# Performance work log

Hardware: AMD Instinct MI355X
Metric: run time of the kernel (lower is better)

The kernel has to match this reference:

```python
import jax, jax.numpy as jnp
import numpy as np


def setup_inputs() -> dict:
    key = jax.random.key(0)
    k1, k2, k3, k4, k5 = jax.random.split(key, 5)
    B, T, H_enc, H_dec, A = 64, 2048, 512, 512, 512
    scale_enc = float(np.sqrt(2.0 / (H_enc + A)))  # xavier_uniform-ish scale
    scale_dec = float(np.sqrt(2.0 / (H_dec + A)))
    scale_v = float(np.sqrt(2.0 / (A + 1)))
    return {
        "encoder_outputs": jax.random.normal(k1, (B, T, H_enc), dtype=jnp.float32),
        "decoder_hidden": jax.random.normal(k2, (B, H_dec), dtype=jnp.float32),
        "W_enc": jax.random.normal(k3, (A, H_enc), dtype=jnp.float32) * scale_enc,
        "W_dec": jax.random.normal(k4, (A, H_dec), dtype=jnp.float32) * scale_dec,
        "V": jax.random.normal(k5, (1, A), dtype=jnp.float32) * scale_v,
    }


def reference(encoder_outputs, decoder_hidden, W_enc, W_dec, V):
    # enc_proj: [B,T,A]; dec_proj: [B,1,A] broadcast-added
    enc_proj = jnp.einsum("bth,ah->bta", encoder_outputs, W_enc)
    dec_proj = jnp.einsum("bh,ah->ba", decoder_hidden, W_dec)[:, None, :]
    energy = jnp.tanh(enc_proj + dec_proj)                      # [B,T,A]
    scores = jnp.einsum("bta,a->bt", energy, V[0])              # [B,T]
    attention_weights = jax.nn.softmax(scores, axis=1)          # [B,T]
    context_vector = jnp.einsum("bt,bth->bh", attention_weights, encoder_outputs)
    return context_vector, attention_weights
```

## Files before the change

kernel.cpp:

```cpp
#include <hip/hip_runtime.h>

#define B_ 64
#define T_ 2048
#define H_ 512
#define A_ 512

typedef unsigned short u16;
typedef __attribute__((ext_vector_type(8))) short bf16x8;
typedef __attribute__((ext_vector_type(4))) float f32x4;

__device__ __forceinline__ u16 f2bf(float f) {
  unsigned u = __float_as_uint(f);
  unsigned r = (u + 0x7FFFu + ((u >> 16) & 1u)) >> 16;
  return (u16)r;
}

__device__ __forceinline__ float bf2f(u16 h) {
  return __uint_as_float(((unsigned)h) << 16);
}

__device__ __forceinline__ float fast_tanh(float x) {
  float e = __expf(2.0f * x);
  return 1.0f - 2.0f * __builtin_amdgcn_rcpf(e + 1.0f);
}

__global__ void k_prep(const float* __restrict__ W, u16* __restrict__ wsB,
                       const float* __restrict__ dec, const float* __restrict__ Wd,
                       float* __restrict__ dp) {
  __shared__ float dl[H_];
  int tid = threadIdx.x;
  int bx = blockIdx.x;
  if (bx < 128) {
    int u = bx * 256 + tid;
    int a = u >> 6;
    int hq = u & 63;
    int ks = hq >> 2;
    int q = hq & 3;
    const float4* src = (const float4*)(W + a * H_ + hq * 8);
    float4 x0 = src[0], x1 = src[1];
    uint4 pk;
    pk.x = (unsigned)f2bf(x0.x) | ((unsigned)f2bf(x0.y) << 16);
    pk.y = (unsigned)f2bf(x0.z) | ((unsigned)f2bf(x0.w) << 16);
    pk.z = (unsigned)f2bf(x1.x) | ((unsigned)f2bf(x1.y) << 16);
    pk.w = (unsigned)f2bf(x1.z) | ((unsigned)f2bf(x1.w) << 16);
    int dst = ks * 2048 + (a >> 4) * 64 + q * 16 + (a & 15);
    ((uint4*)wsB)[dst] = pk;
  } else {
    int e = bx - 128;
    int b = e >> 3;
    int a0 = (e & 7) * 64;
    dl[tid] = dec[b * H_ + tid];
    dl[tid + 256] = dec[b * H_ + tid + 256];
    __syncthreads();
    int al = tid >> 2, p = tid & 3;
    const float4* wr = (const float4*)(Wd + (a0 + al) * H_ + p * 128);
    const float4* dv = (const float4*)(dl + p * 128);
    float s = 0.f;
#pragma unroll 8
    for (int i = 0; i < 32; ++i) {
      float4 w4 = wr[i], d4 = dv[i];
      s += w4.x * d4.x + w4.y * d4.y + w4.z * d4.z + w4.w * d4.w;
    }
    s += __shfl_xor(s, 1);
    s += __shfl_xor(s, 2);
    if (p == 0) dp[b * H_ + a0 + al] = s;
  }
}

__launch_bounds__(512, 4)
__global__ void k_scores(const float* __restrict__ enc, const u16* __restrict__ wsB,
                         const float* __restrict__ dpj, const float* __restrict__ V,
                         float* __restrict__ scores, float* __restrict__ part,
                         float* __restrict__ mz) {
  __shared__ __attribute__((aligned(16))) u16 Ab[64 * 512];
  __shared__ float red[8][64];
  __shared__ float e_lds[64];
  int tid = threadIdx.x;
  int w = tid >> 6, l = tid & 63;
  int q = l >> 4, r = l & 15;
  int m0 = blockIdx.x * 64;
  int b = m0 >> 11;

  int rem = tid & 255;
  int sm = rem >> 6, sq = (rem >> 4) & 3, sr = rem & 15;
  const float* ab = enc + (size_t)(m0 + sm * 16 + sr) * H_ + (tid >> 8) * 32 + sq * 8;

#define STG_WRITE(y0, y1, it)                                         \
  {                                                                   \
    uint4 pk;                                                         \
    pk.x = (unsigned)f2bf(y0.x) | ((unsigned)f2bf(y0.y) << 16);       \
    pk.y = (unsigned)f2bf(y0.z) | ((unsigned)f2bf(y0.w) << 16);       \
    pk.z = (unsigned)f2bf(y1.x) | ((unsigned)f2bf(y1.y) << 16);       \
    pk.w = (unsigned)f2bf(y1.z) | ((unsigned)f2bf(y1.w) << 16);       \
    ((uint4*)Ab)[(it) * 512 + tid] = pk;                              \
  }

  f32x4 acc[4][4];
#pragma unroll
  for (int m = 0; m < 4; ++m)
#pragma unroll
    for (int n = 0; n < 4; ++n) acc[m][n] = (f32x4){0.f, 0.f, 0.f, 0.f};

  const bf16x8* bfrag = (const bf16x8*)wsB;

  {
    float4 y0 = *((const float4*)(ab + 0));
    float4 y1 = *((const float4*)(ab + 4));
    float4 y2 = *((const float4*)(ab + 64));
    float4 y3 = *((const float4*)(ab + 68));
    STG_WRITE(y0, y1, 0)
    STG_WRITE(y2, y3, 1)
  }
  __syncthreads();

#pragma unroll
  for (int c = 0; c < 4; ++c) {
    float4 y0, y1, y2, y3;
    if (c < 3) {
      y0 = *((const float4*)(ab + (2 * c + 2) * 64));
      y1 = *((const float4*)(ab + (2 * c + 2) * 64 + 4));
      y2 = *((const float4*)(ab + (2 * c + 3) * 64));
      y3 = *((const float4*)(ab + (2 * c + 3) * 64 + 4));
    }
#pragma unroll
    for (int kk = 0; kk < 4; ++kk) {
      int ks = c * 4 + kk;
      bf16x8 bb[4], af[4];
#pragma unroll
      for (int n = 0; n < 4; ++n)
        bb[n] = bfrag[ks * 2048 + (w * 4 + n) * 64 + l];
#pragma unroll
      for (int m = 0; m < 4; ++m)
        af[m] = *((const bf16x8*)&Ab[(ks * 256 + m * 64 + l) * 8]);
      __builtin_amdgcn_s_setprio(1);
#pragma unroll
      for (int m = 0; m < 4; ++m)
#pragma unroll
        for (int n = 0; n < 4; ++n)
          acc[m][n] = __builtin_amdgcn_mfma_f32_16x16x32_bf16(af[m], bb[n], acc[m][n], 0, 0, 0);
      __builtin_amdgcn_s_setprio(0);
    }
    if (c < 3) {
      STG_WRITE(y0, y1, 2 * c + 2)
      STG_WRITE(y2, y3, 2 * c + 3)
    }
    __syncthreads();
  }

  float sp[4][4] = {};
  const float* db = dpj + b * A_;
#pragma unroll
  for (int n = 0; n < 4; ++n) {
    int col = w * 64 + n * 16 + r;
    float vv = V[col];
    float dd = db[col];
#pragma unroll
    for (int m = 0; m < 4; ++m)
#pragma unroll
      for (int j = 0; j < 4; ++j)
        sp[m][j] = fmaf(vv, fast_tanh(acc[m][n][j] + dd), sp[m][j]);
  }
#pragma unroll
  for (int m = 0; m < 4; ++m)
#pragma unroll
    for (int j = 0; j < 4; ++j) {
      float v = sp[m][j];
      v += __shfl_xor(v, 1);
      v += __shfl_xor(v, 2);
      v += __shfl_xor(v, 4);
      v += __shfl_xor(v, 8);
      sp[m][j] = v;
    }
  float outv = 0.f;
#pragma unroll
  for (int mm = 0; mm < 4; ++mm)
#pragma unroll
    for (int jj = 0; jj < 4; ++jj)
      if (r == mm * 4 + jj) outv = sp[mm][jj];
  red[w][(r >> 2) * 16 + q * 4 + (r & 3)] = outv;
  __syncthreads();

  if (tid < 64) {
    float s = 0.f;
#pragma unroll
    for (int ww = 0; ww < 8; ++ww) s += red[ww][tid];
    scores[m0 + tid] = s;
    float mx = s;
#pragma unroll
    for (int off = 1; off <= 32; off <<= 1) mx = fmaxf(mx, __shfl_xor(mx, off));
    float e = __expf(s - mx);
    float Z = e;
#pragma unroll
    for (int off = 1; off <= 32; off <<= 1) Z += __shfl_xor(Z, off);
    e_lds[tid] = e;
    if (tid == 0) {
      mz[blockIdx.x * 2] = mx;
      mz[blockIdx.x * 2 + 1] = Z;
    }
  }
  __syncthreads();

  {
    float pv0[8], pv1[8];
#pragma unroll
    for (int j = 0; j < 8; ++j) { pv0[j] = 0.f; pv1[j] = 0.f; }
#pragma unroll
    for (int ksl = 0; ksl < 2; ++ksl) {
      int ks = 2 * w + ksl;
#pragma unroll
      for (int m = 0; m < 4; ++m) {
        uint4 pk = ((const uint4*)Ab)[ks * 256 + m * 64 + l];
        float er = e_lds[m * 16 + r];
        float v0 = bf2f((u16)(pk.x & 0xffff)), v1 = bf2f((u16)(pk.x >> 16));
        float v2 = bf2f((u16)(pk.y & 0xffff)), v3 = bf2f((u16)(pk.y >> 16));
        float v4 = bf2f((u16)(pk.z & 0xffff)), v5 = bf2f((u16)(pk.z >> 16));
        float v6 = bf2f((u16)(pk.w & 0xffff)), v7 = bf2f((u16)(pk.w >> 16));
        if (ksl == 0) {
          pv0[0] = fmaf(er, v0, pv0[0]); pv0[1] = fmaf(er, v1, pv0[1]);
          pv0[2] = fmaf(er, v2, pv0[2]); pv0[3] = fmaf(er, v3, pv0[3]);
          pv0[4] = fmaf(er, v4, pv0[4]); pv0[5] = fmaf(er, v5, pv0[5]);
          pv0[6] = fmaf(er, v6, pv0[6]); pv0[7] = fmaf(er, v7, pv0[7]);
        } else {
          pv1[0] = fmaf(er, v0, pv1[0]); pv1[1] = fmaf(er, v1, pv1[1]);
          pv1[2] = fmaf(er, v2, pv1[2]); pv1[3] = fmaf(er, v3, pv1[3]);
          pv1[4] = fmaf(er, v4, pv1[4]); pv1[5] = fmaf(er, v5, pv1[5]);
          pv1[6] = fmaf(er, v6, pv1[6]); pv1[7] = fmaf(er, v7, pv1[7]);
        }
      }
    }
#pragma unroll
    for (int j = 0; j < 8; ++j) {
      float a0 = pv0[j], a1 = pv1[j];
      a0 += __shfl_xor(a0, 1); a1 += __shfl_xor(a1, 1);
      a0 += __shfl_xor(a0, 2); a1 += __shfl_xor(a1, 2);
      a0 += __shfl_xor(a0, 4); a1 += __shfl_xor(a1, 4);
      a0 += __shfl_xor(a0, 8); a1 += __shfl_xor(a1, 8);
      pv0[j] = a0; pv1[j] = a1;
    }
    float ov = 0.f;
#pragma unroll
    for (int jj = 0; jj < 8; ++jj) {
      if (r == jj) ov = pv0[jj];
      if (r == jj + 8) ov = pv1[jj];
    }
    int col = w * 64 + (r >> 3) * 32 + q * 8 + (r & 7);
    part[(size_t)blockIdx.x * 512 + col] = ov;
  }
#undef STG_WRITE
}

__global__ void k_softmax(const float* __restrict__ scores, float* __restrict__ wts) {
  __shared__ float rm[4], rs[4];
  int b = blockIdx.x, tid = threadIdx.x;
  float s[8];
#pragma unroll
  for (int i = 0; i < 8; ++i) s[i] = scores[b * T_ + i * 256 + tid];
  float mx = s[0];
#pragma unroll
  for (int i = 1; i < 8; ++i) mx = fmaxf(mx, s[i]);
#pragma unroll
  for (int off = 1; off <= 32; off <<= 1) mx = fmaxf(mx, __shfl_xor(mx, off));
  if ((tid & 63) == 0) rm[tid >> 6] = mx;
  __syncthreads();
  mx = fmaxf(fmaxf(rm[0], rm[1]), fmaxf(rm[2], rm[3]));
  float ex[8], se = 0.f;
#pragma unroll
  for (int i = 0; i < 8; ++i) { ex[i] = __expf(s[i] - mx); se += ex[i]; }
#pragma unroll
  for (int off = 1; off <= 32; off <<= 1) se += __shfl_xor(se, off);
  if ((tid & 63) == 0) rs[tid >> 6] = se;
  __syncthreads();
  se = rs[0] + rs[1] + rs[2] + rs[3];
  float inv = 1.0f / se;
#pragma unroll
  for (int i = 0; i < 8; ++i) wts[b * T_ + i * 256 + tid] = ex[i] * inv;
}

__global__ void k_ctx_comb(const float* __restrict__ part, const float* __restrict__ mz,
                           float* __restrict__ ctx) {
  __shared__ float sM[32], sZ[32];
  int b = blockIdx.x, tid = threadIdx.x;
  if (tid < 32) {
    sM[tid] = mz[(b * 32 + tid) * 2];
    sZ[tid] = mz[(b * 32 + tid) * 2 + 1];
  }
  __syncthreads();
  float M = sM[0];
#pragma unroll
  for (int i = 1; i < 32; ++i) M = fmaxf(M, sM[i]);
  float denom = 0.f;
#pragma unroll
  for (int i = 0; i < 32; ++i) denom += sZ[i] * __expf(sM[i] - M);
  float s = 0.f;
#pragma unroll
  for (int i = 0; i < 32; ++i)
    s += part[((size_t)b * 32 + i) * 512 + tid] * __expf(sM[i] - M);
  ctx[b * 512 + tid] = s / denom;
}

extern "C" void kernel_launch(void* const* d_in, const int* in_sizes, int n_in,
                              void* d_out, int out_size, void* d_ws, size_t ws_size,
                              hipStream_t stream) {
  const float* enc  = (const float*)d_in[0];
  const float* dec  = (const float*)d_in[1];
  const float* Wenc = (const float*)d_in[2];
  const float* Wdec = (const float*)d_in[3];
  const float* V    = (const float*)d_in[4];
  float* out = (float*)d_out;
  char* ws = (char*)d_ws;

  u16* wsB      = (u16*)ws;
  float* dpj    = (float*)(ws + 512 * 1024);
  float* scores = (float*)(ws + 640 * 1024);
  float* part   = (float*)(ws + 1152 * 1024);
  float* mz     = (float*)(ws + 1152 * 1024 + 4 * 1024 * 1024);

  float* ctx = out;
  float* wts = out + B_ * H_;

  hipLaunchKernelGGL(k_prep, dim3(640), dim3(256), 0, stream, Wenc, wsB, dec, Wdec, dpj);
  hipLaunchKernelGGL(k_scores, dim3(2048), dim3(512), 0, stream, enc, wsB, dpj, V,
                     scores, part, mz);
  hipLaunchKernelGGL(k_softmax, dim3(64), dim3(256), 0, stream, scores, wts);
  hipLaunchKernelGGL(k_ctx_comb, dim3(64), dim3(512), 0, stream, part, mz, ctx);
}
```

Baseline: 122.8 us.

## Deepen encoder staging prefetch and make all waves compute the softmax tail redundantly

The k_scores main loop now keeps two chunks of encoder loads in flight. Each chunk's global loads are issued two stages ahead of its LDS write, so global latency has more time to hide behind the MFMA work. __syncthreads is replaced with a raw lgkmcnt wait plus s_barrier, which skips waiting on outstanding vector-memory loads. The per-block max/exp reduction is computed redundantly by every wave, and the values are shared by shuffles instead of through an LDS buffer, which removes one barrier. The trade-off is higher register pressure from the extra prefetched float4s and duplicated transcendental work in every wave.

```diff
diff --git a/kernel.cpp b/kernel.cpp
--- a/kernel.cpp
+++ b/kernel.cpp
@@ -23,6 +23,8 @@
   float e = __expf(2.0f * x);
   return 1.0f - 2.0f * __builtin_amdgcn_rcpf(e + 1.0f);
 }
+
+#define BAR_LDS() asm volatile("s_waitcnt lgkmcnt(0)\n\ts_barrier" ::: "memory")
 
 __global__ void k_prep(const float* __restrict__ W, u16* __restrict__ wsB,
                        const float* __restrict__ dec, const float* __restrict__ Wd,
@@ -74,7 +76,6 @@
                          float* __restrict__ mz) {
   __shared__ __attribute__((aligned(16))) u16 Ab[64 * 512];
   __shared__ float red[8][64];
-  __shared__ float e_lds[64];
   int tid = threadIdx.x;
   int w = tid >> 6, l = tid & 63;
   int q = l >> 4, r = l & 15;
@@ -85,6 +86,13 @@
   int sm = rem >> 6, sq = (rem >> 4) & 3, sr = rem & 15;
   const float* ab = enc + (size_t)(m0 + sm * 16 + sr) * H_ + (tid >> 8) * 32 + sq * 8;
 
+#define LOADC(y0, y1, y2, y3, c)                                      \
+  {                                                                   \
+    y0 = *((const float4*)(ab + (2 * (c)) * 64));                     \
+    y1 = *((const float4*)(ab + (2 * (c)) * 64 + 4));                 \
+    y2 = *((const float4*)(ab + (2 * (c) + 1) * 64));                 \
+    y3 = *((const float4*)(ab + (2 * (c) + 1) * 64 + 4));             \
+  }
 #define STG_WRITE(y0, y1, it)                                         \
   {                                                                   \
     uint4 pk;                                                         \
@@ -94,6 +102,28 @@
     pk.w = (unsigned)f2bf(y1.z) | ((unsigned)f2bf(y1.w) << 16);       \
     ((uint4*)Ab)[(it) * 512 + tid] = pk;                              \
   }
+#define WRITEC(y0, y1, y2, y3, c)                                     \
+  {                                                                   \
+    STG_WRITE(y0, y1, 2 * (c))                                        \
+    STG_WRITE(y2, y3, 2 * (c) + 1)                                    \
+  }
+#define COMPUTE4(c)                                                   \
+  {                                                                   \
+    _Pragma("unroll") for (int kk = 0; kk < 4; ++kk) {                \
+      int ks = (c) * 4 + kk;                                          \
+      bf16x8 bb[4], af[4];                                            \
+      _Pragma("unroll") for (int n = 0; n < 4; ++n)                   \
+          bb[n] = bfrag[ks * 2048 + (w * 4 + n) * 64 + l];            \
+      _Pragma("unroll") for (int m = 0; m < 4; ++m)                   \
+          af[m] = *((const bf16x8*)&Ab[(ks * 256 + m * 64 + l) * 8]); \
+      __builtin_amdgcn_s_setprio(1);                                  \
+      _Pragma("unroll") for (int m = 0; m < 4; ++m)                   \
+          _Pragma("unroll") for (int n = 0; n < 4; ++n)               \
+              acc[m][n] = __builtin_amdgcn_mfma_f32_16x16x32_bf16(    \
+                  af[m], bb[n], acc[m][n], 0, 0, 0);                  \
+      __builtin_amdgcn_s_setprio(0);                                  \
+    }                                                                 \
+  }
 
   f32x4 acc[4][4];
 #pragma unroll
@@ -103,49 +133,23 @@
 
   const bf16x8* bfrag = (const bf16x8*)wsB;
 
-  {
-    float4 y0 = *((const float4*)(ab + 0));
-    float4 y1 = *((const float4*)(ab + 4));
-    float4 y2 = *((const float4*)(ab + 64));
-    float4 y3 = *((const float4*)(ab + 68));
-    STG_WRITE(y0, y1, 0)
-    STG_WRITE(y2, y3, 1)
-  }
-  __syncthreads();
-
-#pragma unroll
-  for (int c = 0; c < 4; ++c) {
-    float4 y0, y1, y2, y3;
-    if (c < 3) {
-      y0 = *((const float4*)(ab + (2 * c + 2) * 64));
-      y1 = *((const float4*)(ab + (2 * c + 2) * 64 + 4));
-      y2 = *((const float4*)(ab + (2 * c + 3) * 64));
-      y3 = *((const float4*)(ab + (2 * c + 3) * 64 + 4));
-    }
-#pragma unroll
-    for (int kk = 0; kk < 4; ++kk) {
-      int ks = c * 4 + kk;
-      bf16x8 bb[4], af[4];
-#pragma unroll
-      for (int n = 0; n < 4; ++n)
-        bb[n] = bfrag[ks * 2048 + (w * 4 + n) * 64 + l];
-#pragma unroll
-      for (int m = 0; m < 4; ++m)
-        af[m] = *((const bf16x8*)&Ab[(ks * 256 + m * 64 + l) * 8]);
-      __builtin_amdgcn_s_setprio(1);
-#pragma unroll
-      for (int m = 0; m < 4; ++m)
-#pragma unroll
-        for (int n = 0; n < 4; ++n)
-          acc[m][n] = __builtin_amdgcn_mfma_f32_16x16x32_bf16(af[m], bb[n], acc[m][n], 0, 0, 0);
-      __builtin_amdgcn_s_setprio(0);
-    }
-    if (c < 3) {
-      STG_WRITE(y0, y1, 2 * c + 2)
-      STG_WRITE(y2, y3, 2 * c + 3)
-    }
-    __syncthreads();
-  }
+  float4 ya0, ya1, ya2, ya3, yb0, yb1, yb2, yb3;
+  LOADC(ya0, ya1, ya2, ya3, 0)
+  LOADC(yb0, yb1, yb2, yb3, 1)
+  WRITEC(ya0, ya1, ya2, ya3, 0)
+  BAR_LDS();
+  LOADC(ya0, ya1, ya2, ya3, 2)
+  COMPUTE4(0)
+  WRITEC(yb0, yb1, yb2, yb3, 1)
+  BAR_LDS();
+  LOADC(yb0, yb1, yb2, yb3, 3)
+  COMPUTE4(1)
+  WRITEC(ya0, ya1, ya2, ya3, 2)
+  BAR_LDS();
+  COMPUTE4(2)
+  WRITEC(yb0, yb1, yb2, yb3, 3)
+  BAR_LDS();
+  COMPUTE4(3)
 
   float sp[4][4] = {};
   const float* db = dpj + b * A_;
@@ -178,27 +182,26 @@
     for (int jj = 0; jj < 4; ++jj)
       if (r == mm * 4 + jj) outv = sp[mm][jj];
   red[w][(r >> 2) * 16 + q * 4 + (r & 3)] = outv;
-  __syncthreads();
-
-  if (tid < 64) {
-    float s = 0.f;
-#pragma unroll
-    for (int ww = 0; ww < 8; ++ww) s += red[ww][tid];
-    scores[m0 + tid] = s;
-    float mx = s;
-#pragma unroll
-    for (int off = 1; off <= 32; off <<= 1) mx = fmaxf(mx, __shfl_xor(mx, off));
-    float e = __expf(s - mx);
-    float Z = e;
-#pragma unroll
-    for (int off = 1; off <= 32; off <<= 1) Z += __shfl_xor(Z, off);
-    e_lds[tid] = e;
-    if (tid == 0) {
-      mz[blockIdx.x * 2] = mx;
-      mz[blockIdx.x * 2 + 1] = Z;
-    }
-  }
-  __syncthreads();
+  BAR_LDS();
+
+  float s = 0.f;
+#pragma unroll
+  for (int ww = 0; ww < 8; ++ww) s += red[ww][l];
+  if (w == 0) scores[m0 + l] = s;
+  float mx = s;
+#pragma unroll
+  for (int off = 1; off <= 32; off <<= 1) mx = fmaxf(mx, __shfl_xor(mx, off));
+  float e = __expf(s - mx);
+  float Z = e;
+#pragma unroll
+  for (int off = 1; off <= 32; off <<= 1) Z += __shfl_xor(Z, off);
+  if (tid == 0) {
+    mz[blockIdx.x * 2] = mx;
+    mz[blockIdx.x * 2 + 1] = Z;
+  }
+  float em[4];
+#pragma unroll
+  for (int m = 0; m < 4; ++m) em[m] = __shfl(e, m * 16 + r);
 
   {
     float pv0[8], pv1[8];
@@ -210,7 +213,7 @@
 #pragma unroll
       for (int m = 0; m < 4; ++m) {
         uint4 pk = ((const uint4*)Ab)[ks * 256 + m * 64 + l];
-        float er = e_lds[m * 16 + r];
+        float er = em[m];
         float v0 = bf2f((u16)(pk.x & 0xffff)), v1 = bf2f((u16)(pk.x >> 16));
         float v2 = bf2f((u16)(pk.y & 0xffff)), v3 = bf2f((u16)(pk.y >> 16));
         float v4 = bf2f((u16)(pk.z & 0xffff)), v5 = bf2f((u16)(pk.z >> 16));
@@ -246,7 +249,10 @@
     int col = w * 64 + (r >> 3) * 32 + q * 8 + (r & 7);
     part[(size_t)blockIdx.x * 512 + col] = ov;
   }
+#undef LOADC
 #undef STG_WRITE
+#undef WRITEC
+#undef COMPUTE4
 }
 
 __global__ void k_softmax(const float* __restrict__ scores, float* __restrict__ wts) {
```

Result: no change. 122.0 us (-0.7%).
